# Kernel optimization log

Hardware: AMD Instinct MI355X
Metric: run time of the kernel (lower is better)

Reference implementation:

```python
import jax, jax.numpy as jnp
import numpy as np


def setup_inputs() -> dict:
    key = jax.random.key(0)
    ks = jax.random.split(key, 6)
    B, L, N, C, D = 8, 512, 2048, 1024, 128
    return {
        "teacher_logits": jax.random.normal(ks[0], (B, L, N), dtype=jnp.float32),
        "teacher_features": jax.random.normal(ks[1], (B, N, C), dtype=jnp.float32),
        "Wq": jax.random.normal(ks[2], (D, C), dtype=jnp.float32) * (1.0 / np.sqrt(C)),
        "bq": jnp.zeros((D,), dtype=jnp.float32),
        "Wk": jax.random.normal(ks[3], (D, C), dtype=jnp.float32) * (1.0 / np.sqrt(C)),
        "bk": jnp.zeros((D,), dtype=jnp.float32),
    }


def reference(teacher_logits, teacher_features, Wq, bq, Wk, bk):
    # Linear projections (torch nn.Linear: x @ W^T + b)
    query = jnp.einsum("bnc,dc->bnd", teacher_features, Wq) + bq  # [B,N,D]
    key = jnp.einsum("bnc,dc->bnd", teacher_features, Wk) + bk    # [B,N,D]
    energy = jnp.einsum("bnd,bmd->bnm", query, key)               # [B,N,N]
    attention = jax.nn.softmax(energy, axis=-1)                   # softmax over last dim
    # x_m = teacher_logits @ attention^T : [B,L,N] x [B,N,N]^T -> [B,L,N]
    x_m = jnp.einsum("bln,bmn->blm", teacher_logits, attention)
    return x_m
```

## Files before the change

kernel.cpp:

```cpp
#include <hip/hip_runtime.h>
#include <hip/hip_bf16.h>

#define B_ 8
#define L_ 512
#define N_ 2048
#define C_ 1024
#define D_ 128

typedef __attribute__((ext_vector_type(8))) short    short8;
typedef __attribute__((ext_vector_type(8))) _Float16 half8;
typedef __attribute__((ext_vector_type(4))) float    floatx4;

static __device__ __forceinline__ float s2f(short s) {
    return __uint_as_float(((unsigned)(unsigned short)s) << 16);
}
static __device__ __forceinline__ short f2bf(float f) {
    union { __hip_bfloat16 h; short s; } u;
    u.h = __float2bfloat16(f);
    return u.s;
}

struct F8 { float v[8]; };

static __device__ __forceinline__ F8 load8(const void* raw, long off, int is_bf16) {
    F8 r;
    if (is_bf16) {
        short8 x = *reinterpret_cast<const short8*>((const short*)raw + off);
        #pragma unroll
        for (int i = 0; i < 8; ++i) r.v[i] = s2f(x[i]);
    } else {
        const float* p = (const float*)raw + off;
        float4 a = *reinterpret_cast<const float4*>(p);
        float4 b = *reinterpret_cast<const float4*>(p + 4);
        r.v[0]=a.x; r.v[1]=a.y; r.v[2]=a.z; r.v[3]=a.w;
        r.v[4]=b.x; r.v[5]=b.y; r.v[6]=b.z; r.v[7]=b.w;
    }
    return r;
}

static __device__ __forceinline__ float bias_at(const void* raw, int d, int is_bf16) {
    return is_bf16 ? s2f(((const short*)raw)[d]) : ((const float*)raw)[d];
}

static __device__ __forceinline__ void load_lds16(const void* g, void* l) {
    __builtin_amdgcn_global_load_lds(
        (const __attribute__((address_space(1))) void*)g,
        (__attribute__((address_space(3))) void*)l, 16, 0, 0);
}

__global__ void detect_kernel(const unsigned* __restrict__ words, int* __restrict__ flag) {
    int cnt = 0;
    for (int i = threadIdx.x; i < 256; i += 64) {
        float lowv = __uint_as_float(words[i] << 16);
        float a = fabsf(lowv);
        if (a >= 1e-5f && a <= 100.0f) cnt++;
    }
    #pragma unroll
    for (int off = 32; off; off >>= 1) cnt += __shfl_down(cnt, off);
    if (threadIdx.x == 0) flag[0] = (cnt > 128) ? 1 : 0;
}

__global__ __launch_bounds__(256) void cvt_kernel(const void* __restrict__ in_raw,
                                                  short* __restrict__ out, long n,
                                                  const int* __restrict__ flag) {
    const int is_bf16 = *flag;
    long i = ((long)blockIdx.x * 256 + threadIdx.x) * 8;
    if (i >= n) return;
    F8 x = load8(in_raw, i, is_bf16);
    short8 o;
    #pragma unroll
    for (int j = 0; j < 8; ++j) o[j] = f2bf(x.v[j]);
    *reinterpret_cast<short8*>(out + i) = o;
}

__global__ __launch_bounds__(256) void cvt_half_kernel(const void* __restrict__ in_raw,
                                                       _Float16* __restrict__ out, long n,
                                                       const int* __restrict__ flag) {
    const int is_bf16 = *flag;
    long i = ((long)blockIdx.x * 256 + threadIdx.x) * 8;
    if (i >= n) return;
    F8 x = load8(in_raw, i, is_bf16);
    half8 o;
    #pragma unroll
    for (int j = 0; j < 8; ++j) o[j] = (_Float16)x.v[j];
    *reinterpret_cast<half8*>(out + i) = o;
}

__global__ __launch_bounds__(512) void proj_kernel(
    const void* __restrict__ Fraw,
    const _Float16* __restrict__ Wq_h,
    const void* __restrict__ bq_raw,
    const _Float16* __restrict__ Wk_h,
    const void* __restrict__ bk_raw,
    _Float16* __restrict__ Q, _Float16* __restrict__ K,
    const int* __restrict__ flag)
{
    const int is_bf16 = *flag;
    const int tid  = threadIdx.x;
    const int wave = tid >> 6;
    const int lane = tid & 63;
    const int quad = lane >> 4;
    const int l16  = lane & 15;
    const long r0  = (long)blockIdx.x * 128;

    const bool isK = (blockIdx.y != 0);
    const _Float16* W = isK ? Wk_h : Wq_h;
    const void* braw  = isK ? bk_raw : bq_raw;
    _Float16* Out     = isK ? K : Q;

    const int m0 = (wave & 3) * 32;
    const int n0 = (wave >> 2) * 64;

    __shared__ _Float16 Ft[128 * 32];
    __shared__ _Float16 Wt[128 * 32];

    floatx4 acc[2][4] = {};

    const int frow  = tid >> 2;
    const int fkoff = (tid & 3) * 8;
    const int wsrow  = lane >> 2;
    const int wskoff = (lane & 3) * 8;

    for (int kb = 0; kb < 32; ++kb) {
        const int k0 = kb * 32;

        load_lds16(W + (long)(wave * 16 + wsrow) * C_ + k0 + wskoff,
                   Wt + wave * 512 + lane * 8);

        {
            F8 x = load8(Fraw, (r0 + frow) * (long)C_ + k0 + fkoff, is_bf16);
            half8 h;
            #pragma unroll
            for (int j = 0; j < 8; ++j) h[j] = (_Float16)x.v[j];
            *reinterpret_cast<half8*>(Ft + tid * 8) = h;
        }
        __syncthreads();

        half8 af[2], bf[4];
        #pragma unroll
        for (int t = 0; t < 2; ++t)
            af[t] = *reinterpret_cast<const half8*>(Ft + (m0 + t * 16 + l16) * 32 + quad * 8);
        #pragma unroll
        for (int u = 0; u < 4; ++u)
            bf[u] = *reinterpret_cast<const half8*>(Wt + (n0 + u * 16 + l16) * 32 + quad * 8);

        #pragma unroll
        for (int t = 0; t < 2; ++t)
            #pragma unroll
            for (int u = 0; u < 4; ++u)
                acc[t][u] = __builtin_amdgcn_mfma_f32_16x16x32_f16(af[t], bf[u], acc[t][u], 0, 0, 0);

        __syncthreads();
    }

    #pragma unroll
    for (int u = 0; u < 4; ++u) {
        const int d = n0 + u * 16 + l16;
        const float bv = bias_at(braw, d, is_bf16);
        #pragma unroll
        for (int t = 0; t < 2; ++t)
            #pragma unroll
            for (int r = 0; r < 4; ++r) {
                const long row = r0 + m0 + t * 16 + quad * 4 + r;
                Out[row * D_ + d] = (_Float16)(acc[t][u][r] + bv);
            }
    }
}

__global__ __launch_bounds__(512) void attn_kernel(
    const _Float16* __restrict__ Q,
    const _Float16* __restrict__ K,
    short* __restrict__ A)
{
    const int b    = blockIdx.y;
    const int i0   = blockIdx.x * 32;
    const int wave = threadIdx.x >> 6;
    const int lane = threadIdx.x & 63;
    const int quad = lane >> 4;
    const int l16  = lane & 15;

    const _Float16* Qb = Q + (long)b * N_ * D_;
    const _Float16* Kb = K + (long)b * N_ * D_;

    half8 a[2][4];
    #pragma unroll
    for (int v = 0; v < 2; ++v)
        #pragma unroll
        for (int s = 0; s < 4; ++s)
            a[v][s] = *reinterpret_cast<const half8*>(
                Qb + (long)(i0 + v * 16 + l16) * D_ + s * 32 + quad * 8);

    floatx4 acc[2][16];
    #pragma unroll
    for (int v = 0; v < 2; ++v)
        #pragma unroll
        for (int t = 0; t < 16; ++t) acc[v][t] = (floatx4){0.f, 0.f, 0.f, 0.f};

    const int jbase = wave * 256;
    #pragma unroll
    for (int t = 0; t < 16; ++t) {
        const _Float16* krow = Kb + (long)(jbase + t * 16 + l16) * D_ + quad * 8;
        #pragma unroll
        for (int s = 0; s < 4; ++s) {
            half8 kf = *reinterpret_cast<const half8*>(krow + s * 32);
            acc[0][t] = __builtin_amdgcn_mfma_f32_16x16x32_f16(a[0][s], kf, acc[0][t], 0, 0, 0);
            acc[1][t] = __builtin_amdgcn_mfma_f32_16x16x32_f16(a[1][s], kf, acc[1][t], 0, 0, 0);
        }
    }

    __shared__ float red[32][8];
    float gmax[2][4], inv[2][4];

    #pragma unroll
    for (int v = 0; v < 2; ++v)
        #pragma unroll
        for (int r = 0; r < 4; ++r) {
            float m = -1e30f;
            #pragma unroll
            for (int t = 0; t < 16; ++t) m = fmaxf(m, acc[v][t][r]);
            m = fmaxf(m, __shfl_xor(m, 1));
            m = fmaxf(m, __shfl_xor(m, 2));
            m = fmaxf(m, __shfl_xor(m, 4));
            m = fmaxf(m, __shfl_xor(m, 8));
            if (l16 == 0) red[v * 16 + quad * 4 + r][wave] = m;
        }
    __syncthreads();
    #pragma unroll
    for (int v = 0; v < 2; ++v)
        #pragma unroll
        for (int r = 0; r < 4; ++r) {
            float m = red[v * 16 + quad * 4 + r][0];
            #pragma unroll
            for (int w = 1; w < 8; ++w) m = fmaxf(m, red[v * 16 + quad * 4 + r][w]);
            gmax[v][r] = m;
        }
    __syncthreads();

    #pragma unroll
    for (int v = 0; v < 2; ++v)
        #pragma unroll
        for (int r = 0; r < 4; ++r) {
            float s = 0.f;
            #pragma unroll
            for (int t = 0; t < 16; ++t) {
                float e = __expf(acc[v][t][r] - gmax[v][r]);
                acc[v][t][r] = e;
                s += e;
            }
            s += __shfl_xor(s, 1);
            s += __shfl_xor(s, 2);
            s += __shfl_xor(s, 4);
            s += __shfl_xor(s, 8);
            if (l16 == 0) red[v * 16 + quad * 4 + r][wave] = s;
        }
    __syncthreads();
    #pragma unroll
    for (int v = 0; v < 2; ++v)
        #pragma unroll
        for (int r = 0; r < 4; ++r) {
            float s = 0.f;
            #pragma unroll
            for (int w = 0; w < 8; ++w) s += red[v * 16 + quad * 4 + r][w];
            inv[v][r] = 1.0f / s;
        }

    short* Ab = A + (long)b * N_ * N_;
    #pragma unroll
    for (int v = 0; v < 2; ++v)
        #pragma unroll
        for (int t = 0; t < 16; ++t) {
            const int j = jbase + t * 16 + l16;
            #pragma unroll
            for (int r = 0; r < 4; ++r) {
                Ab[(long)(i0 + v * 16 + quad * 4 + r) * N_ + j] =
                    f2bf(acc[v][t][r] * inv[v][r]);
            }
        }
}

__global__ __launch_bounds__(256) void xm_kernel(
    const short* __restrict__ Lg,
    const short* __restrict__ A,
    void* __restrict__ OutRaw,
    const int* __restrict__ flag)
{
    const int is_bf16 = *flag;
    const int b  = blockIdx.z;
    const int r0 = blockIdx.x * 128;
    const int c0 = blockIdx.y * 128;
    const int wave = threadIdx.x >> 6;
    const int lane = threadIdx.x & 63;
    const int quad = lane >> 4;
    const int l16  = lane & 15;

    __shared__ short Atile[128 * 32];
    __shared__ short Btile[128 * 32];

    const short* Lb = Lg + (long)b * L_ * N_;
    const short* Ab = A  + (long)b * N_ * N_;

    const int m0 = (wave & 1) * 64;
    const int n0 = (wave >> 1) * 64;

    floatx4 acc[4][4] = {};

    const int srow  = lane >> 2;
    const int skoff = (lane & 3) * 8;

    for (int kb = 0; kb < 64; ++kb) {
        const int k0 = kb * 32;
        #pragma unroll
        for (int j = 0; j < 4; ++j) {
            const int cc = wave * 4 + j;
            if (cc < 8) {
                const short* src = Lb + (long)(r0 + cc * 16 + srow) * N_ + k0 + skoff;
                load_lds16(src, Atile + cc * 512);
            } else {
                const int c8 = cc - 8;
                const short* src = Ab + (long)(c0 + c8 * 16 + srow) * N_ + k0 + skoff;
                load_lds16(src, Btile + c8 * 512);
            }
        }
        __syncthreads();

        short8 af[4], bf[4];
        #pragma unroll
        for (int t = 0; t < 4; ++t)
            af[t] = *reinterpret_cast<const short8*>(Atile + (m0 + t * 16 + l16) * 32 + quad * 8);
        #pragma unroll
        for (int u = 0; u < 4; ++u)
            bf[u] = *reinterpret_cast<const short8*>(Btile + (n0 + u * 16 + l16) * 32 + quad * 8);

        #pragma unroll
        for (int t = 0; t < 4; ++t)
            #pragma unroll
            for (int u = 0; u < 4; ++u)
                acc[t][u] = __builtin_amdgcn_mfma_f32_16x16x32_bf16(af[t], bf[u], acc[t][u], 0, 0, 0);

        __syncthreads();
    }

    if (is_bf16) {
        short* Ob = (short*)OutRaw + (long)b * L_ * N_;
        #pragma unroll
        for (int t = 0; t < 4; ++t)
            #pragma unroll
            for (int u = 0; u < 4; ++u)
                #pragma unroll
                for (int r = 0; r < 4; ++r) {
                    const long row = r0 + m0 + t * 16 + quad * 4 + r;
                    const int  col = c0 + n0 + u * 16 + l16;
                    Ob[row * N_ + col] = f2bf(acc[t][u][r]);
                }
    } else {
        float* Ob = (float*)OutRaw + (long)b * L_ * N_;
        #pragma unroll
        for (int t = 0; t < 4; ++t)
            #pragma unroll
            for (int u = 0; u < 4; ++u)
                #pragma unroll
                for (int r = 0; r < 4; ++r) {
                    const long row = r0 + m0 + t * 16 + quad * 4 + r;
                    const int  col = c0 + n0 + u * 16 + l16;
                    Ob[row * N_ + col] = acc[t][u][r];
                }
    }
}

extern "C" void kernel_launch(void* const* d_in, const int* in_sizes, int n_in,
                              void* d_out, int out_size, void* d_ws, size_t ws_size,
                              hipStream_t stream) {
    const void* logits_raw = d_in[0];
    const void* feats_raw  = d_in[1];
    const void* wq_raw     = d_in[2];
    const void* bq_raw     = d_in[3];
    const void* wk_raw     = d_in[4];
    const void* bk_raw     = d_in[5];

    char* ws = (char*)d_ws;
    size_t off = 0;
    int* flag = (int*)(ws + off);           off += 256;
    short* logb = (short*)(ws + off);       off += (size_t)B_ * L_ * N_ * 2;
    _Float16* Wq_h = (_Float16*)(ws + off); off += (size_t)D_ * C_ * 2;
    _Float16* Wk_h = (_Float16*)(ws + off); off += (size_t)D_ * C_ * 2;
    _Float16* Q = (_Float16*)(ws + off);    off += (size_t)B_ * N_ * D_ * 2;
    _Float16* K = (_Float16*)(ws + off);    off += (size_t)B_ * N_ * D_ * 2;
    short* A = (short*)(ws + off);          off += (size_t)B_ * N_ * N_ * 2;

    hipLaunchKernelGGL(detect_kernel, dim3(1), dim3(64), 0, stream,
                       (const unsigned*)feats_raw, flag);
    hipLaunchKernelGGL(cvt_kernel, dim3((B_ * L_ * N_) / (256 * 8)), dim3(256), 0, stream,
                       logits_raw, logb, (long)B_ * L_ * N_, flag);
    hipLaunchKernelGGL(cvt_half_kernel, dim3((D_ * C_) / (256 * 8)), dim3(256), 0, stream,
                       wq_raw, Wq_h, (long)D_ * C_, flag);
    hipLaunchKernelGGL(cvt_half_kernel, dim3((D_ * C_) / (256 * 8)), dim3(256), 0, stream,
                       wk_raw, Wk_h, (long)D_ * C_, flag);
    hipLaunchKernelGGL(proj_kernel, dim3(B_ * N_ / 128, 2), dim3(512), 0, stream,
                       feats_raw, Wq_h, bq_raw, Wk_h, bk_raw, Q, K, flag);
    hipLaunchKernelGGL(attn_kernel, dim3(N_ / 32, B_), dim3(512), 0, stream,
                       Q, K, A);
    hipLaunchKernelGGL(xm_kernel, dim3(L_ / 128, N_ / 128, B_), dim3(256), 0, stream,
                       logb, A, d_out, flag);
}
```

Measured before the change: 285.4 us.

## Skip conversions for bf16 inputs, retile projection, widen attention block, deepen xm K-tile

The conversion kernels now exit early when the inputs are detected as bf16. The projection kernel and the xm kernel then read the raw bf16 data directly, using bf16 MFMA, instead of going through converted copies. The projection kernel moves to 64-row tiles with 256 threads, and the attention kernel uses 1024 threads with each wave covering 128 columns. The xm kernel doubles its K tile to 64 so it synchronises half as often, in exchange for more LDS per block. The aim is to cut the conversion passes and the extra memory traffic they cause, at some cost to occupancy in the wider kernels.

Result: no change. 288.4 us (+1.1%).

```diff
diff --git a/kernel.cpp b/kernel.cpp
--- a/kernel.cpp
+++ b/kernel.cpp
@@ -63,10 +63,10 @@
 __global__ __launch_bounds__(256) void cvt_kernel(const void* __restrict__ in_raw,
                                                   short* __restrict__ out, long n,
                                                   const int* __restrict__ flag) {
-    const int is_bf16 = *flag;
+    if (*flag) return;
     long i = ((long)blockIdx.x * 256 + threadIdx.x) * 8;
     if (i >= n) return;
-    F8 x = load8(in_raw, i, is_bf16);
+    F8 x = load8(in_raw, i, 0);
     short8 o;
     #pragma unroll
     for (int j = 0; j < 8; ++j) o[j] = f2bf(x.v[j]);
@@ -76,22 +76,21 @@
 __global__ __launch_bounds__(256) void cvt_half_kernel(const void* __restrict__ in_raw,
                                                        _Float16* __restrict__ out, long n,
                                                        const int* __restrict__ flag) {
-    const int is_bf16 = *flag;
+    if (*flag) return;
     long i = ((long)blockIdx.x * 256 + threadIdx.x) * 8;
     if (i >= n) return;
-    F8 x = load8(in_raw, i, is_bf16);
+    F8 x = load8(in_raw, i, 0);
     half8 o;
     #pragma unroll
     for (int j = 0; j < 8; ++j) o[j] = (_Float16)x.v[j];
     *reinterpret_cast<half8*>(out + i) = o;
 }
 
-__global__ __launch_bounds__(512) void proj_kernel(
+__global__ __launch_bounds__(256) void proj_kernel(
     const void* __restrict__ Fraw,
-    const _Float16* __restrict__ Wq_h,
-    const void* __restrict__ bq_raw,
-    const _Float16* __restrict__ Wk_h,
-    const void* __restrict__ bk_raw,
+    const void* __restrict__ Wq_raw, const void* __restrict__ Wk_raw,
+    const _Float16* __restrict__ Wq_h, const _Float16* __restrict__ Wk_h,
+    const void* __restrict__ bq_raw, const void* __restrict__ bk_raw,
     _Float16* __restrict__ Q, _Float16* __restrict__ K,
     const int* __restrict__ flag)
 {
@@ -101,56 +100,85 @@
     const int lane = tid & 63;
     const int quad = lane >> 4;
     const int l16  = lane & 15;
-    const long r0  = (long)blockIdx.x * 128;
+    const long r0  = (long)blockIdx.x * 64;
 
     const bool isK = (blockIdx.y != 0);
-    const _Float16* W = isK ? Wk_h : Wq_h;
-    const void* braw  = isK ? bk_raw : bq_raw;
-    _Float16* Out     = isK ? K : Q;
-
-    const int m0 = (wave & 3) * 32;
-    const int n0 = (wave >> 2) * 64;
-
-    __shared__ _Float16 Ft[128 * 32];
-    __shared__ _Float16 Wt[128 * 32];
+    const void* braw = isK ? bk_raw : bq_raw;
+    _Float16* Out    = isK ? K : Q;
+
+    const int m0 = (wave & 1) * 32;
+    const int n0 = (wave >> 1) * 64;
+
+    __shared__ short Ft[64 * 32];
+    __shared__ short Wt[128 * 32];
 
     floatx4 acc[2][4] = {};
 
-    const int frow  = tid >> 2;
-    const int fkoff = (tid & 3) * 8;
-    const int wsrow  = lane >> 2;
-    const int wskoff = (lane & 3) * 8;
-
-    for (int kb = 0; kb < 32; ++kb) {
-        const int k0 = kb * 32;
-
-        load_lds16(W + (long)(wave * 16 + wsrow) * C_ + k0 + wskoff,
-                   Wt + wave * 512 + lane * 8);
-
-        {
-            F8 x = load8(Fraw, (r0 + frow) * (long)C_ + k0 + fkoff, is_bf16);
-            half8 h;
-            #pragma unroll
-            for (int j = 0; j < 8; ++j) h[j] = (_Float16)x.v[j];
-            *reinterpret_cast<half8*>(Ft + tid * 8) = h;
-        }
-        __syncthreads();
-
-        half8 af[2], bf[4];
-        #pragma unroll
-        for (int t = 0; t < 2; ++t)
-            af[t] = *reinterpret_cast<const half8*>(Ft + (m0 + t * 16 + l16) * 32 + quad * 8);
-        #pragma unroll
-        for (int u = 0; u < 4; ++u)
-            bf[u] = *reinterpret_cast<const half8*>(Wt + (n0 + u * 16 + l16) * 32 + quad * 8);
-
-        #pragma unroll
-        for (int t = 0; t < 2; ++t)
+    const int srow  = lane >> 2;
+    const int skoff = (lane & 3) * 8;
+
+    if (is_bf16) {
+        const short* Fr = (const short*)Fraw;
+        const short* Wr = (const short*)(isK ? Wk_raw : Wq_raw);
+        for (int kb = 0; kb < 32; ++kb) {
+            const int k0 = kb * 32;
+            load_lds16(Fr + (r0 + wave * 16 + srow) * (long)C_ + k0 + skoff,
+                       Ft + wave * 512 + lane * 8);
+            #pragma unroll
+            for (int jj = 0; jj < 2; ++jj) {
+                load_lds16(Wr + (long)(wave * 32 + jj * 16 + srow) * C_ + k0 + skoff,
+                           Wt + (wave * 2 + jj) * 512 + lane * 8);
+            }
+            __syncthreads();
+
+            short8 af[2], bfr[4];
+            #pragma unroll
+            for (int t = 0; t < 2; ++t)
+                af[t] = *reinterpret_cast<const short8*>(Ft + (m0 + t * 16 + l16) * 32 + quad * 8);
             #pragma unroll
             for (int u = 0; u < 4; ++u)
-                acc[t][u] = __builtin_amdgcn_mfma_f32_16x16x32_f16(af[t], bf[u], acc[t][u], 0, 0, 0);
-
-        __syncthreads();
+                bfr[u] = *reinterpret_cast<const short8*>(Wt + (n0 + u * 16 + l16) * 32 + quad * 8);
+            #pragma unroll
+            for (int t = 0; t < 2; ++t)
+                #pragma unroll
+                for (int u = 0; u < 4; ++u)
+                    acc[t][u] = __builtin_amdgcn_mfma_f32_16x16x32_bf16(af[t], bfr[u], acc[t][u], 0, 0, 0);
+            __syncthreads();
+        }
+    } else {
+        const _Float16* Wh = isK ? Wk_h : Wq_h;
+        _Float16* Fth = (_Float16*)Ft;
+        _Float16* Wth = (_Float16*)Wt;
+        for (int kb = 0; kb < 32; ++kb) {
+            const int k0 = kb * 32;
+            #pragma unroll
+            for (int jj = 0; jj < 2; ++jj) {
+                load_lds16(Wh + (long)(wave * 32 + jj * 16 + srow) * C_ + k0 + skoff,
+                           Wth + (wave * 2 + jj) * 512 + lane * 8);
+            }
+            {
+                F8 x = load8(Fraw, (r0 + (tid >> 2)) * (long)C_ + k0 + (tid & 3) * 8, 0);
+                half8 h;
+                #pragma unroll
+                for (int j = 0; j < 8; ++j) h[j] = (_Float16)x.v[j];
+                *reinterpret_cast<half8*>(Fth + tid * 8) = h;
+            }
+            __syncthreads();
+
+            half8 af[2], bfr[4];
+            #pragma unroll
+            for (int t = 0; t < 2; ++t)
+                af[t] = *reinterpret_cast<const half8*>(Fth + (m0 + t * 16 + l16) * 32 + quad * 8);
+            #pragma unroll
+            for (int u = 0; u < 4; ++u)
+                bfr[u] = *reinterpret_cast<const half8*>(Wth + (n0 + u * 16 + l16) * 32 + quad * 8);
+            #pragma unroll
+            for (int t = 0; t < 2; ++t)
+                #pragma unroll
+                for (int u = 0; u < 4; ++u)
+                    acc[t][u] = __builtin_amdgcn_mfma_f32_16x16x32_f16(af[t], bfr[u], acc[t][u], 0, 0, 0);
+            __syncthreads();
+        }
     }
 
     #pragma unroll
@@ -167,7 +195,7 @@
     }
 }
 
-__global__ __launch_bounds__(512) void attn_kernel(
+__global__ __launch_bounds__(1024) void attn_kernel(
     const _Float16* __restrict__ Q,
     const _Float16* __restrict__ K,
     short* __restrict__ A)
@@ -190,15 +218,15 @@
             a[v][s] = *reinterpret_cast<const half8*>(
                 Qb + (long)(i0 + v * 16 + l16) * D_ + s * 32 + quad * 8);
 
-    floatx4 acc[2][16];
-    #pragma unroll
-    for (int v = 0; v < 2; ++v)
-        #pragma unroll
-        for (int t = 0; t < 16; ++t) acc[v][t] = (floatx4){0.f, 0.f, 0.f, 0.f};
-
-    const int jbase = wave * 256;
-    #pragma unroll
-    for (int t = 0; t < 16; ++t) {
+    floatx4 acc[2][8];
+    #pragma unroll
+    for (int v = 0; v < 2; ++v)
+        #pragma unroll
+        for (int t = 0; t < 8; ++t) acc[v][t] = (floatx4){0.f, 0.f, 0.f, 0.f};
+
+    const int jbase = wave * 128;
+    #pragma unroll
+    for (int t = 0; t < 8; ++t) {
         const _Float16* krow = Kb + (long)(jbase + t * 16 + l16) * D_ + quad * 8;
         #pragma unroll
         for (int s = 0; s < 4; ++s) {
@@ -208,7 +236,7 @@
         }
     }
 
-    __shared__ float red[32][8];
+    __shared__ float red[32][16];
     float gmax[2][4], inv[2][4];
 
     #pragma unroll
@@ -217,7 +245,7 @@
         for (int r = 0; r < 4; ++r) {
             float m = -1e30f;
             #pragma unroll
-            for (int t = 0; t < 16; ++t) m = fmaxf(m, acc[v][t][r]);
+            for (int t = 0; t < 8; ++t) m = fmaxf(m, acc[v][t][r]);
             m = fmaxf(m, __shfl_xor(m, 1));
             m = fmaxf(m, __shfl_xor(m, 2));
             m = fmaxf(m, __shfl_xor(m, 4));
@@ -231,7 +259,7 @@
         for (int r = 0; r < 4; ++r) {
             float m = red[v * 16 + quad * 4 + r][0];
             #pragma unroll
-            for (int w = 1; w < 8; ++w) m = fmaxf(m, red[v * 16 + quad * 4 + r][w]);
+            for (int w = 1; w < 16; ++w) m = fmaxf(m, red[v * 16 + quad * 4 + r][w]);
             gmax[v][r] = m;
         }
     __syncthreads();
@@ -242,7 +270,7 @@
         for (int r = 0; r < 4; ++r) {
             float s = 0.f;
             #pragma unroll
-            for (int t = 0; t < 16; ++t) {
+            for (int t = 0; t < 8; ++t) {
                 float e = __expf(acc[v][t][r] - gmax[v][r]);
                 acc[v][t][r] = e;
                 s += e;
@@ -260,7 +288,7 @@
         for (int r = 0; r < 4; ++r) {
             float s = 0.f;
             #pragma unroll
-            for (int w = 0; w < 8; ++w) s += red[v * 16 + quad * 4 + r][w];
+            for (int w = 0; w < 16; ++w) s += red[v * 16 + quad * 4 + r][w];
             inv[v][r] = 1.0f / s;
         }
 
@@ -268,7 +296,7 @@
     #pragma unroll
     for (int v = 0; v < 2; ++v)
         #pragma unroll
-        for (int t = 0; t < 16; ++t) {
+        for (int t = 0; t < 8; ++t) {
             const int j = jbase + t * 16 + l16;
             #pragma unroll
             for (int r = 0; r < 4; ++r) {
@@ -279,7 +307,8 @@
 }
 
 __global__ __launch_bounds__(256) void xm_kernel(
-    const short* __restrict__ Lg,
+    const void* __restrict__ Lraw,
+    const short* __restrict__ Lcvt,
     const short* __restrict__ A,
     void* __restrict__ OutRaw,
     const int* __restrict__ flag)
@@ -293,50 +322,53 @@
     const int quad = lane >> 4;
     const int l16  = lane & 15;
 
-    __shared__ short Atile[128 * 32];
-    __shared__ short Btile[128 * 32];
-
-    const short* Lb = Lg + (long)b * L_ * N_;
-    const short* Ab = A  + (long)b * N_ * N_;
+    __shared__ short Atile[128 * 64];
+    __shared__ short Btile[128 * 64];
+
+    const short* Lb = (is_bf16 ? (const short*)Lraw : Lcvt) + (long)b * L_ * N_;
+    const short* Ab = A + (long)b * N_ * N_;
 
     const int m0 = (wave & 1) * 64;
     const int n0 = (wave >> 1) * 64;
 
     floatx4 acc[4][4] = {};
 
-    const int srow  = lane >> 2;
-    const int skoff = (lane & 3) * 8;
-
-    for (int kb = 0; kb < 64; ++kb) {
-        const int k0 = kb * 32;
-        #pragma unroll
-        for (int j = 0; j < 4; ++j) {
-            const int cc = wave * 4 + j;
-            if (cc < 8) {
-                const short* src = Lb + (long)(r0 + cc * 16 + srow) * N_ + k0 + skoff;
+    const int srow  = lane >> 3;
+    const int skoff = (lane & 7) * 8;
+
+    for (int kb = 0; kb < 32; ++kb) {
+        const int k0 = kb * 64;
+        #pragma unroll
+        for (int j = 0; j < 8; ++j) {
+            const int cc = wave * 8 + j;
+            if (cc < 16) {
+                const short* src = Lb + (long)(r0 + cc * 8 + srow) * N_ + k0 + skoff;
                 load_lds16(src, Atile + cc * 512);
             } else {
-                const int c8 = cc - 8;
-                const short* src = Ab + (long)(c0 + c8 * 16 + srow) * N_ + k0 + skoff;
+                const int c8 = cc - 16;
+                const short* src = Ab + (long)(c0 + c8 * 8 + srow) * N_ + k0 + skoff;
                 load_lds16(src, Btile + c8 * 512);
             }
         }
         __syncthreads();
 
-        short8 af[4], bf[4];
-        #pragma unroll
-        for (int t = 0; t < 4; ++t)
-            af[t] = *reinterpret_cast<const short8*>(Atile + (m0 + t * 16 + l16) * 32 + quad * 8);
-        #pragma unroll
-        for (int u = 0; u < 4; ++u)
-            bf[u] = *reinterpret_cast<const short8*>(Btile + (n0 + u * 16 + l16) * 32 + quad * 8);
-
-        #pragma unroll
-        for (int t = 0; t < 4; ++t)
+        #pragma unroll
+        for (int ks = 0; ks < 2; ++ks) {
+            short8 af[4], bf[4];
+            #pragma unroll
+            for (int t = 0; t < 4; ++t)
+                af[t] = *reinterpret_cast<const short8*>(
+                    Atile + (m0 + t * 16 + l16) * 64 + ks * 32 + quad * 8);
             #pragma unroll
             for (int u = 0; u < 4; ++u)
-                acc[t][u] = __builtin_amdgcn_mfma_f32_16x16x32_bf16(af[t], bf[u], acc[t][u], 0, 0, 0);
-
+                bf[u] = *reinterpret_cast<const short8*>(
+                    Btile + (n0 + u * 16 + l16) * 64 + ks * 32 + quad * 8);
+            #pragma unroll
+            for (int t = 0; t < 4; ++t)
+                #pragma unroll
+                for (int u = 0; u < 4; ++u)
+                    acc[t][u] = __builtin_amdgcn_mfma_f32_16x16x32_bf16(af[t], bf[u], acc[t][u], 0, 0, 0);
+        }
         __syncthreads();
     }
 
@@ -395,10 +427,10 @@
                        wq_raw, Wq_h, (long)D_ * C_, flag);
     hipLaunchKernelGGL(cvt_half_kernel, dim3((D_ * C_) / (256 * 8)), dim3(256), 0, stream,
                        wk_raw, Wk_h, (long)D_ * C_, flag);
-    hipLaunchKernelGGL(proj_kernel, dim3(B_ * N_ / 128, 2), dim3(512), 0, stream,
-                       feats_raw, Wq_h, bq_raw, Wk_h, bk_raw, Q, K, flag);
-    hipLaunchKernelGGL(attn_kernel, dim3(N_ / 32, B_), dim3(512), 0, stream,
+    hipLaunchKernelGGL(proj_kernel, dim3(B_ * N_ / 64, 2), dim3(256), 0, stream,
+                       feats_raw, wq_raw, wk_raw, Wq_h, Wk_h, bq_raw, bk_raw, Q, K, flag);
+    hipLaunchKernelGGL(attn_kernel, dim3(N_ / 32, B_), dim3(1024), 0, stream,
                        Q, K, A);
     hipLaunchKernelGGL(xm_kernel, dim3(L_ / 128, N_ / 128, B_), dim3(256), 0, stream,
-                       logb, A, d_out, flag);
-}
+                       logits_raw, logb, A, d_out, flag);
+}
```
